# Performance work log

Measured on AMD Instinct MI355X. Metric: run time of the kernel, lower is better.

The kernel has to match this reference:

```python
import jax, jax.numpy as jnp
import numpy as np

N_TOKENS = 262144
IN_DIM = 512
NUM_EXPERTS = 64
D_E = 64
TOP_K = 2
EPS = 1e-12  # torch F.normalize eps


def _l2norm(x, axis):
    n = jnp.linalg.norm(x, axis=axis, keepdims=True)
    return x / jnp.maximum(n, EPS)


def setup_inputs() -> dict:
    key = jax.random.key(0)
    k_h, k_w, k_e, k_svd = jax.random.split(key, 4)
    h = jax.random.normal(k_h, (N_TOKENS, IN_DIM), dtype=jnp.float32)
    # xavier_uniform for W [d_e, in_dim]
    limit = float(np.sqrt(6.0 / (D_E + IN_DIM)))
    W = jax.random.uniform(k_w, (D_E, IN_DIM), minval=-limit, maxval=limit, dtype=jnp.float32)
    # orthonormal expert embeddings (SVD of random matrix), scaled by init_expert_norm=0.1
    M = jax.random.normal(k_svd, (D_E, D_E), dtype=jnp.float32)
    U, _, _ = jnp.linalg.svd(M)
    expert_embeddings = U[:NUM_EXPERTS, :] * 0.1
    tau = jnp.array(1.0, dtype=jnp.float32)
    return {"h": h, "W": W, "expert_embeddings": expert_embeddings, "tau": tau}


def reference(h, W, expert_embeddings, tau):
    # projection: [N, d_e]
    h_proj = h @ W.T
    h_norm = _l2norm(h_proj, axis=1)
    e_norm = _l2norm(expert_embeddings, axis=1)
    # cosine scores: [N, E]
    scores = h_norm @ e_norm.T
    full_gates = jax.nn.softmax(scores / tau, axis=1)
    topk_values, topk_indices = jax.lax.top_k(full_gates, TOP_K)
    normalized_topk = jax.nn.softmax(topk_values, axis=1)
    rows = jnp.arange(full_gates.shape[0])[:, None]
    sparse_gates = jnp.zeros_like(full_gates).at[rows, topk_indices].set(normalized_topk)
    return sparse_gates, topk_indices, full_gates
```

## Files before the change

kernel.cpp:

```cpp
#include <hip/hip_runtime.h>
#include <math.h>

#define NT 262144
#define KD 512
#define NE 64
#define DE 64

constexpr int BM = 128;
constexpr int NS = KD / 32;
constexpr int WS_EN = 49152;
constexpr int LD2 = 68;

using f32x4 = __attribute__((ext_vector_type(4))) float;
using s16x8 = __attribute__((ext_vector_type(8))) short;

typedef const __attribute__((address_space(1))) unsigned int* gp1_t;
typedef __attribute__((address_space(3))) unsigned int* lp3_t;

__device__ __forceinline__ void split8(float4 lo, float4 hi,
                                       s16x8& o1, s16x8& o2, s16x8& o3) {
    float x[8] = {lo.x, lo.y, lo.z, lo.w, hi.x, hi.y, hi.z, hi.w};
    union { unsigned int u[4]; s16x8 v; } r1, r2, r3;
    #pragma unroll
    for (int p = 0; p < 4; ++p) {
        float f0 = x[2 * p], f1 = x[2 * p + 1];
        unsigned int a = __float_as_uint(f0), b = __float_as_uint(f1);
        unsigned int a1 = a & 0xFFFF0000u, b1 = b & 0xFFFF0000u;
        r1.u[p] = (a1 >> 16) | b1;
        float q0 = f0 - __uint_as_float(a1);
        float q1 = f1 - __uint_as_float(b1);
        unsigned int a2 = __float_as_uint(q0) & 0xFFFF0000u;
        unsigned int b2 = __float_as_uint(q1) & 0xFFFF0000u;
        r2.u[p] = (a2 >> 16) | b2;
        float s0 = q0 - __uint_as_float(a2);
        float s1 = q1 - __uint_as_float(b2);
        r3.u[p] = (__float_as_uint(s0) >> 16) | (__float_as_uint(s1) & 0xFFFF0000u);
    }
    o1 = r1.v; o2 = r2.v; o3 = r3.v;
}

__device__ __forceinline__ s16x8 ld_frag(const unsigned int* p) {
    union { uint4 q; s16x8 v; } u;
    u.q = *(const uint4*)p;
    return u.v;
}

__global__ void prep(const float* __restrict__ W, const float* __restrict__ E,
                     unsigned int* __restrict__ ws) {
    const int tid = threadIdx.x;
    if (blockIdx.x < 16) {
        const int idx = blockIdx.x * 256 + tid;
        const int row = idx >> 6, k8 = idx & 63;
        const float* src = W + (size_t)row * KD + k8 * 8;
        float4 lo = *(const float4*)src, hi = *(const float4*)(src + 4);
        s16x8 o1, o2, o3;
        split8(lo, hi, o1, o2, o3);
        union { s16x8 v; uint4 q; } u1, u2, u3;
        u1.v = o1; u2.v = o2; u3.v = o3;
        const int ks = k8 >> 2, lk = k8 & 3, ct = row >> 4, lr = row & 15;
        const int g = ks * 4 + ct, lane = lk * 16 + lr;
        unsigned int* base = ws + (size_t)g * 768 + lane * 4;
        *(uint4*)(base)       = u1.q;
        *(uint4*)(base + 256) = u2.q;
        *(uint4*)(base + 512) = u3.q;
    } else {
        const int er = tid >> 2, part = tid & 3;
        float ss = 0.f;
        float4 ev[4];
        #pragma unroll
        for (int u = 0; u < 4; ++u) {
            ev[u] = *(const float4*)(E + er * DE + part * 16 + u * 4);
            ss = fmaf(ev[u].x, ev[u].x, ss);
            ss = fmaf(ev[u].y, ev[u].y, ss);
            ss = fmaf(ev[u].z, ev[u].z, ss);
            ss = fmaf(ev[u].w, ev[u].w, ss);
        }
        ss += __shfl_xor(ss, 1, 64);
        ss += __shfl_xor(ss, 2, 64);
        const float inv_e = 1.0f / fmaxf(sqrtf(ss), 1e-12f);
        #pragma unroll
        for (int u = 0; u < 4; ++u) {
            ev[u].x *= inv_e; ev[u].y *= inv_e; ev[u].z *= inv_e; ev[u].w *= inv_e;
        }
        #pragma unroll
        for (int half = 0; half < 2; ++half) {
            const int d0 = part * 16 + half * 8;
            s16x8 o1, o2, o3;
            split8(ev[half * 2], ev[half * 2 + 1], o1, o2, o3);
            union { s16x8 v; uint4 q; } u1, u2, u3;
            u1.v = o1; u2.v = o2; u3.v = o3;
            const int k2 = d0 >> 5, kg = (d0 >> 3) & 3;
            const int ge = k2 * 4 + (er >> 4), l = (er & 15) | (kg << 4);
            unsigned int* base = ws + WS_EN + (size_t)ge * 768 + l * 4;
            *(uint4*)(base)       = u1.q;
            *(uint4*)(base + 256) = u2.q;
            *(uint4*)(base + 512) = u3.q;
        }
    }
}

__global__ __launch_bounds__(256, 4) void moe_all(const float* __restrict__ h,
                                                  const unsigned int* __restrict__ wsW,
                                                  const float* __restrict__ tau_p,
                                                  float* __restrict__ out) {
    __shared__ float smem[10240];

    const int tid = threadIdx.x;
    const int lane = tid & 63;
    const int wv = tid >> 6;
    const int lr = lane & 15;
    const int lk = lane >> 4;
    const long tok0 = (long)blockIdx.x * BM;

    f32x4 acc[2][4];
    #pragma unroll
    for (int rt = 0; rt < 2; ++rt)
        #pragma unroll
        for (int ct = 0; ct < 4; ++ct)
            acc[rt][ct] = (f32x4){0.f, 0.f, 0.f, 0.f};

#define STAGE_A(KS)                                                            \
    {                                                                          \
        _Pragma("unroll")                                                      \
        for (int n = 0; n < 4; ++n) {                                          \
            const int flat = (wv * 4 + n) * 64 + lane;                         \
            const int t = flat >> 3, q = flat & 7;                             \
            const int qs = q ^ (t & 7);                                        \
            const float* g = h + (tok0 + t) * (long)KD + (KS) * 32 + qs * 4;   \
            float* l = smem + 6144 + wv * 1024 + n * 256;                      \
            __builtin_amdgcn_global_load_lds((gp1_t)(const void*)g,            \
                                             (lp3_t)(void*)l, 16, 0, 0);       \
        }                                                                      \
    }

#define STAGE_B(CUR, KS)                                                       \
    {                                                                          \
        _Pragma("unroll")                                                      \
        for (int i = 0; i < 3; ++i) {                                          \
            const unsigned int* g = wsW + (size_t)(KS) * 3072 + i * 1024       \
                                    + wv * 256 + lane * 4;                     \
            float* l = smem + (CUR) * 3072 + i * 1024 + wv * 256;              \
            __builtin_amdgcn_global_load_lds((gp1_t)(const void*)g,            \
                                             (lp3_t)(void*)l, 16, 0, 0);       \
        }                                                                      \
    }

    STAGE_B(0, 0);
    STAGE_A(0);

    const int sw = lr & 7;
    const int q0 = (lk * 2) ^ sw;
    const int q1 = (lk * 2 + 1) ^ sw;
    const float* abase = smem + 6144 + wv * 1024;

    for (int ks = 0; ks < NS; ++ks) {
        const int cur = ks & 1;
        asm volatile("s_waitcnt vmcnt(0)" ::: "memory");
        __builtin_amdgcn_s_barrier();
        if (ks + 1 < NS) { STAGE_B(cur ^ 1, ks + 1); }
        __builtin_amdgcn_sched_barrier(0);

        float4 xl0 = *(const float4*)(abase + lr * 32 + q0 * 4);
        float4 xh0 = *(const float4*)(abase + lr * 32 + q1 * 4);
        float4 xl1 = *(const float4*)(abase + (lr + 16) * 32 + q0 * 4);
        float4 xh1 = *(const float4*)(abase + (lr + 16) * 32 + q1 * 4);
        asm volatile("s_waitcnt lgkmcnt(0)" ::: "memory");
        if (ks + 1 < NS) { STAGE_A(ks + 1); }
        __builtin_amdgcn_sched_barrier(0);

        s16x8 a1[2], a2[2], a3[2];
        split8(xl0, xh0, a1[0], a2[0], a3[0]);
        split8(xl1, xh1, a1[1], a2[1], a3[1]);

        #pragma unroll
        for (int ct = 0; ct < 4; ++ct) {
            const unsigned int* bb =
                (const unsigned int*)(smem + cur * 3072 + ct * 768) + lane * 4;
            s16x8 b1 = ld_frag(bb);
            s16x8 b2 = ld_frag(bb + 256);
            s16x8 b3 = ld_frag(bb + 512);
            f32x4 c0 = acc[0][ct], c1 = acc[1][ct];
            c0 = __builtin_amdgcn_mfma_f32_16x16x32_bf16(a1[0], b1, c0, 0, 0, 0);
            c1 = __builtin_amdgcn_mfma_f32_16x16x32_bf16(a1[1], b1, c1, 0, 0, 0);
            c0 = __builtin_amdgcn_mfma_f32_16x16x32_bf16(a2[0], b1, c0, 0, 0, 0);
            c1 = __builtin_amdgcn_mfma_f32_16x16x32_bf16(a2[1], b1, c1, 0, 0, 0);
            c0 = __builtin_amdgcn_mfma_f32_16x16x32_bf16(a1[0], b2, c0, 0, 0, 0);
            c1 = __builtin_amdgcn_mfma_f32_16x16x32_bf16(a1[1], b2, c1, 0, 0, 0);
            c0 = __builtin_amdgcn_mfma_f32_16x16x32_bf16(a3[0], b1, c0, 0, 0, 0);
            c1 = __builtin_amdgcn_mfma_f32_16x16x32_bf16(a3[1], b1, c1, 0, 0, 0);
            c0 = __builtin_amdgcn_mfma_f32_16x16x32_bf16(a2[0], b2, c0, 0, 0, 0);
            c1 = __builtin_amdgcn_mfma_f32_16x16x32_bf16(a2[1], b2, c1, 0, 0, 0);
            c0 = __builtin_amdgcn_mfma_f32_16x16x32_bf16(a1[0], b3, c0, 0, 0, 0);
            c1 = __builtin_amdgcn_mfma_f32_16x16x32_bf16(a1[1], b3, c1, 0, 0, 0);
            acc[0][ct] = c0; acc[1][ct] = c1;
        }
    }

    float inv_n[2][4];
    #pragma unroll
    for (int rt = 0; rt < 2; ++rt) {
        #pragma unroll
        for (int r = 0; r < 4; ++r) {
            float ss = 0.f;
            #pragma unroll
            for (int ct = 0; ct < 4; ++ct)
                ss = fmaf(acc[rt][ct][r], acc[rt][ct][r], ss);
            ss += __shfl_xor(ss, 1, 64);
            ss += __shfl_xor(ss, 2, 64);
            ss += __shfl_xor(ss, 4, 64);
            ss += __shfl_xor(ss, 8, 64);
            inv_n[rt][r] = 1.0f / fmaxf(sqrtf(ss), 1e-12f);
        }
    }

    __syncthreads();

    #pragma unroll
    for (int rt = 0; rt < 2; ++rt)
        #pragma unroll
        for (int ct = 0; ct < 4; ++ct)
            #pragma unroll
            for (int r = 0; r < 4; ++r) {
                const int t = wv * 32 + rt * 16 + lk * 4 + r;
                smem[t * LD2 + ct * 16 + lr] = acc[rt][ct][r] * inv_n[rt][r];
            }

    const unsigned int* wsE = wsW + WS_EN;
    f32x4 sc[2][4];
    #pragma unroll
    for (int rt = 0; rt < 2; ++rt)
        #pragma unroll
        for (int ce = 0; ce < 4; ++ce)
            sc[rt][ce] = (f32x4){0.f, 0.f, 0.f, 0.f};

    #pragma unroll
    for (int k2 = 0; k2 < 2; ++k2) {
        s16x8 ha1[2], ha2[2], ha3[2];
        #pragma unroll
        for (int rt = 0; rt < 2; ++rt) {
            const float* ra = smem + (wv * 32 + rt * 16 + lr) * LD2 + k2 * 32 + lk * 8;
            float4 lo = *(const float4*)ra;
            float4 hi = *(const float4*)(ra + 4);
            split8(lo, hi, ha1[rt], ha2[rt], ha3[rt]);
        }
        #pragma unroll
        for (int ce = 0; ce < 4; ++ce) {
            const unsigned int* bb = wsE + (k2 * 4 + ce) * 768 + lane * 4;
            s16x8 b1 = ld_frag(bb);
            s16x8 b2 = ld_frag(bb + 256);
            s16x8 b3 = ld_frag(bb + 512);
            #pragma unroll
            for (int rt = 0; rt < 2; ++rt) {
                f32x4 c = sc[rt][ce];
                c = __builtin_amdgcn_mfma_f32_16x16x32_bf16(ha1[rt], b1, c, 0, 0, 0);
                c = __builtin_amdgcn_mfma_f32_16x16x32_bf16(ha2[rt], b1, c, 0, 0, 0);
                c = __builtin_amdgcn_mfma_f32_16x16x32_bf16(ha1[rt], b2, c, 0, 0, 0);
                c = __builtin_amdgcn_mfma_f32_16x16x32_bf16(ha3[rt], b1, c, 0, 0, 0);
                c = __builtin_amdgcn_mfma_f32_16x16x32_bf16(ha2[rt], b2, c, 0, 0, 0);
                c = __builtin_amdgcn_mfma_f32_16x16x32_bf16(ha1[rt], b3, c, 0, 0, 0);
                sc[rt][ce] = c;
            }
        }
    }

    const float inv_tau = 1.0f / tau_p[0];
    float* outS = out;
    float* outI = out + (size_t)NT * 64;
    float* outF = out + (size_t)NT * 66;

    #pragma unroll
    for (int rt = 0; rt < 2; ++rt) {
        #pragma unroll
        for (int r = 0; r < 4; ++r) {
            const long tok = tok0 + wv * 32 + rt * 16 + lk * 4 + r;
            float s[4];
            #pragma unroll
            for (int ce = 0; ce < 4; ++ce) s[ce] = sc[rt][ce][r] * inv_tau;

            float m = fmaxf(fmaxf(s[0], s[1]), fmaxf(s[2], s[3]));
            m = fmaxf(m, __shfl_xor(m, 1, 64));
            m = fmaxf(m, __shfl_xor(m, 2, 64));
            m = fmaxf(m, __shfl_xor(m, 4, 64));
            m = fmaxf(m, __shfl_xor(m, 8, 64));

            float g[4], z = 0.f;
            #pragma unroll
            for (int ce = 0; ce < 4; ++ce) { g[ce] = __expf(s[ce] - m); z += g[ce]; }
            z += __shfl_xor(z, 1, 64);
            z += __shfl_xor(z, 2, 64);
            z += __shfl_xor(z, 4, 64);
            z += __shfl_xor(z, 8, 64);
            const float invZ = 1.0f / z;

            #pragma unroll
            for (int ce = 0; ce < 4; ++ce)
                outF[tok * 64 + ce * 16 + lr] = g[ce] * invZ;

            float v1 = -3.4e38f, v2 = -3.4e38f;
            int i1 = 1 << 20, i2 = 1 << 20;
            #pragma unroll
            for (int ce = 0; ce < 4; ++ce) {
                float v = s[ce];
                int e = ce * 16 + lr;
                if (v > v1 || (v == v1 && e < i1)) { v2 = v1; i2 = i1; v1 = v; i1 = e; }
                else if (v > v2 || (v == v2 && e < i2)) { v2 = v; i2 = e; }
            }
            #pragma unroll
            for (int msk = 1; msk <= 8; msk <<= 1) {
                float o1 = __shfl_xor(v1, msk, 64); int oi1 = __shfl_xor(i1, msk, 64);
                float o2 = __shfl_xor(v2, msk, 64); int oi2 = __shfl_xor(i2, msk, 64);
                if (o1 > v1 || (o1 == v1 && oi1 < i1)) {
                    if (v1 > o2 || (v1 == o2 && i1 < oi2)) { v2 = v1; i2 = i1; }
                    else { v2 = o2; i2 = oi2; }
                    v1 = o1; i1 = oi1;
                } else {
                    if (o1 > v2 || (o1 == v2 && oi1 < i2)) { v2 = o1; i2 = oi1; }
                }
            }

            float gv1 = __expf(v1 - m) * invZ;
            float gv2 = __expf(v2 - m) * invZ;
            float qq = __expf(gv2 - gv1);
            float w1 = 1.0f / (1.0f + qq);
            float w2 = qq * w1;

            #pragma unroll
            for (int ce = 0; ce < 4; ++ce) {
                int e = ce * 16 + lr;
                outS[tok * 64 + e] = (e == i1) ? w1 : ((e == i2) ? w2 : 0.0f);
            }
            if (lr == 0) {
                *(float2*)(outI + tok * 2) = make_float2((float)i1, (float)i2);
            }
        }
    }
#undef STAGE_A
#undef STAGE_B
}

extern "C" void kernel_launch(void* const* d_in, const int* in_sizes, int n_in,
                              void* d_out, int out_size, void* d_ws, size_t ws_size,
                              hipStream_t stream) {
    const float* h   = (const float*)d_in[0];
    const float* W   = (const float*)d_in[1];
    const float* E   = (const float*)d_in[2];
    const float* tau = (const float*)d_in[3];
    float* out = (float*)d_out;
    unsigned int* ws = (unsigned int*)d_ws;

    prep<<<17, 256, 0, stream>>>(W, E, ws);
    moe_all<<<NT / BM, 256, 0, stream>>>(h, ws, tau, out);
}
```

Before: 170.2 us.

## Single-buffer W tiles and reuse LDS per wave to raise occupancy

The W-fragment stage goes from double-buffered to single-buffered, with a second barrier before each refill, and the loop is rewritten as macro phases with finer vmcnt waits. The normalized projection is staged through a small per-wave LDS region in two halves, so shared memory drops from 40 KB to 28 KB and launch bounds rise from 4 to 5 blocks per CU. It also adds s_setprio around the MFMA blocks and hoists the tau load to kernel start. The intent is better latency hiding through higher occupancy, at the cost of an extra barrier per K step and less overlap of W loads. The padded stride of 33 also makes the float4 LDS reads misaligned.

```diff
diff --git a/kernel.cpp b/kernel.cpp
--- a/kernel.cpp
+++ b/kernel.cpp
@@ -9,7 +9,7 @@
 constexpr int BM = 128;
 constexpr int NS = KD / 32;
 constexpr int WS_EN = 49152;
-constexpr int LD2 = 68;
+constexpr int LT = 33;
 
 using f32x4 = __attribute__((ext_vector_type(4))) float;
 using s16x8 = __attribute__((ext_vector_type(8))) short;
@@ -99,11 +99,11 @@
     }
 }
 
-__global__ __launch_bounds__(256, 4) void moe_all(const float* __restrict__ h,
+__global__ __launch_bounds__(256, 5) void moe_all(const float* __restrict__ h,
                                                   const unsigned int* __restrict__ wsW,
                                                   const float* __restrict__ tau_p,
                                                   float* __restrict__ out) {
-    __shared__ float smem[10240];
+    __shared__ float smem[7168];
 
     const int tid = threadIdx.x;
     const int lane = tid & 63;
@@ -111,6 +111,9 @@
     const int lr = lane & 15;
     const int lk = lane >> 4;
     const long tok0 = (long)blockIdx.x * BM;
+
+    const float inv_tau_pre = 1.0f / tau_p[0];
+    asm volatile("s_waitcnt vmcnt(0)" ::: "memory");
 
     f32x4 acc[2][4];
     #pragma unroll
@@ -127,74 +130,81 @@
             const int t = flat >> 3, q = flat & 7;                             \
             const int qs = q ^ (t & 7);                                        \
             const float* g = h + (tok0 + t) * (long)KD + (KS) * 32 + qs * 4;   \
-            float* l = smem + 6144 + wv * 1024 + n * 256;                      \
+            float* l = smem + 3072 + wv * 1024 + n * 256;                      \
             __builtin_amdgcn_global_load_lds((gp1_t)(const void*)g,            \
                                              (lp3_t)(void*)l, 16, 0, 0);       \
         }                                                                      \
     }
 
-#define STAGE_B(CUR, KS)                                                       \
+#define STAGE_B(KS)                                                            \
     {                                                                          \
         _Pragma("unroll")                                                      \
         for (int i = 0; i < 3; ++i) {                                          \
             const unsigned int* g = wsW + (size_t)(KS) * 3072 + i * 1024       \
                                     + wv * 256 + lane * 4;                     \
-            float* l = smem + (CUR) * 3072 + i * 1024 + wv * 256;              \
+            float* l = smem + i * 1024 + wv * 256;                             \
             __builtin_amdgcn_global_load_lds((gp1_t)(const void*)g,            \
                                              (lp3_t)(void*)l, 16, 0, 0);       \
         }                                                                      \
     }
 
-    STAGE_B(0, 0);
+#define PHASE(KS, LAST)                                                        \
+    {                                                                          \
+        asm volatile("s_waitcnt vmcnt(3)" ::: "memory");     \
+        float4 xl0 = *(const float4*)(abase + lr * 32 + q0 * 4);               \
+        float4 xh0 = *(const float4*)(abase + lr * 32 + q1 * 4);               \
+        float4 xl1 = *(const float4*)(abase + (lr + 16) * 32 + q0 * 4);        \
+        float4 xh1 = *(const float4*)(abase + (lr + 16) * 32 + q1 * 4);        \
+        asm volatile("s_waitcnt lgkmcnt(0)" ::: "memory");     \
+        if (!(LAST)) { STAGE_A((KS) + 1); }                                    \
+        __builtin_amdgcn_sched_barrier(0);                                     \
+        s16x8 a1[2], a2[2], a3[2];                                             \
+        split8(xl0, xh0, a1[0], a2[0], a3[0]);                                 \
+        split8(xl1, xh1, a1[1], a2[1], a3[1]);                                 \
+        if (LAST) { asm volatile("s_waitcnt vmcnt(0)" ::: "memory"); }         \
+        else      { asm volatile("s_waitcnt vmcnt(4)" ::: "memory"); }         \
+        __builtin_amdgcn_s_barrier();             \
+        __builtin_amdgcn_s_setprio(1);                                         \
+        _Pragma("unroll")                                                      \
+        for (int ct = 0; ct < 4; ++ct) {                                       \
+            const unsigned int* bb =                                           \
+                (const unsigned int*)(smem + ct * 768) + lane * 4;             \
+            s16x8 b1 = ld_frag(bb);                                            \
+            s16x8 b2 = ld_frag(bb + 256);                                      \
+            s16x8 b3 = ld_frag(bb + 512);                                      \
+            f32x4 c0 = acc[0][ct], c1 = acc[1][ct];                            \
+            c0 = __builtin_amdgcn_mfma_f32_16x16x32_bf16(a1[0], b1, c0, 0, 0, 0); \
+            c1 = __builtin_amdgcn_mfma_f32_16x16x32_bf16(a1[1], b1, c1, 0, 0, 0); \
+            c0 = __builtin_amdgcn_mfma_f32_16x16x32_bf16(a2[0], b1, c0, 0, 0, 0); \
+            c1 = __builtin_amdgcn_mfma_f32_16x16x32_bf16(a2[1], b1, c1, 0, 0, 0); \
+            c0 = __builtin_amdgcn_mfma_f32_16x16x32_bf16(a1[0], b2, c0, 0, 0, 0); \
+            c1 = __builtin_amdgcn_mfma_f32_16x16x32_bf16(a1[1], b2, c1, 0, 0, 0); \
+            c0 = __builtin_amdgcn_mfma_f32_16x16x32_bf16(a3[0], b1, c0, 0, 0, 0); \
+            c1 = __builtin_amdgcn_mfma_f32_16x16x32_bf16(a3[1], b1, c1, 0, 0, 0); \
+            c0 = __builtin_amdgcn_mfma_f32_16x16x32_bf16(a2[0], b2, c0, 0, 0, 0); \
+            c1 = __builtin_amdgcn_mfma_f32_16x16x32_bf16(a2[1], b2, c1, 0, 0, 0); \
+            c0 = __builtin_amdgcn_mfma_f32_16x16x32_bf16(a1[0], b3, c0, 0, 0, 0); \
+            c1 = __builtin_amdgcn_mfma_f32_16x16x32_bf16(a1[1], b3, c1, 0, 0, 0); \
+            acc[0][ct] = c0; acc[1][ct] = c1;                                  \
+        }                                                                      \
+        __builtin_amdgcn_s_setprio(0);                                         \
+        if (!(LAST)) {                                                         \
+            __builtin_amdgcn_s_barrier();        \
+            STAGE_B((KS) + 1);                          \
+        }                                                                      \
+    }
+
     STAGE_A(0);
+    STAGE_B(0);
+    __builtin_amdgcn_sched_barrier(0);
 
     const int sw = lr & 7;
     const int q0 = (lk * 2) ^ sw;
     const int q1 = (lk * 2 + 1) ^ sw;
-    const float* abase = smem + 6144 + wv * 1024;
-
-    for (int ks = 0; ks < NS; ++ks) {
-        const int cur = ks & 1;
-        asm volatile("s_waitcnt vmcnt(0)" ::: "memory");
-        __builtin_amdgcn_s_barrier();
-        if (ks + 1 < NS) { STAGE_B(cur ^ 1, ks + 1); }
-        __builtin_amdgcn_sched_barrier(0);
-
-        float4 xl0 = *(const float4*)(abase + lr * 32 + q0 * 4);
-        float4 xh0 = *(const float4*)(abase + lr * 32 + q1 * 4);
-        float4 xl1 = *(const float4*)(abase + (lr + 16) * 32 + q0 * 4);
-        float4 xh1 = *(const float4*)(abase + (lr + 16) * 32 + q1 * 4);
-        asm volatile("s_waitcnt lgkmcnt(0)" ::: "memory");
-        if (ks + 1 < NS) { STAGE_A(ks + 1); }
-        __builtin_amdgcn_sched_barrier(0);
-
-        s16x8 a1[2], a2[2], a3[2];
-        split8(xl0, xh0, a1[0], a2[0], a3[0]);
-        split8(xl1, xh1, a1[1], a2[1], a3[1]);
-
-        #pragma unroll
-        for (int ct = 0; ct < 4; ++ct) {
-            const unsigned int* bb =
-                (const unsigned int*)(smem + cur * 3072 + ct * 768) + lane * 4;
-            s16x8 b1 = ld_frag(bb);
-            s16x8 b2 = ld_frag(bb + 256);
-            s16x8 b3 = ld_frag(bb + 512);
-            f32x4 c0 = acc[0][ct], c1 = acc[1][ct];
-            c0 = __builtin_amdgcn_mfma_f32_16x16x32_bf16(a1[0], b1, c0, 0, 0, 0);
-            c1 = __builtin_amdgcn_mfma_f32_16x16x32_bf16(a1[1], b1, c1, 0, 0, 0);
-            c0 = __builtin_amdgcn_mfma_f32_16x16x32_bf16(a2[0], b1, c0, 0, 0, 0);
-            c1 = __builtin_amdgcn_mfma_f32_16x16x32_bf16(a2[1], b1, c1, 0, 0, 0);
-            c0 = __builtin_amdgcn_mfma_f32_16x16x32_bf16(a1[0], b2, c0, 0, 0, 0);
-            c1 = __builtin_amdgcn_mfma_f32_16x16x32_bf16(a1[1], b2, c1, 0, 0, 0);
-            c0 = __builtin_amdgcn_mfma_f32_16x16x32_bf16(a3[0], b1, c0, 0, 0, 0);
-            c1 = __builtin_amdgcn_mfma_f32_16x16x32_bf16(a3[1], b1, c1, 0, 0, 0);
-            c0 = __builtin_amdgcn_mfma_f32_16x16x32_bf16(a2[0], b2, c0, 0, 0, 0);
-            c1 = __builtin_amdgcn_mfma_f32_16x16x32_bf16(a2[1], b2, c1, 0, 0, 0);
-            c0 = __builtin_amdgcn_mfma_f32_16x16x32_bf16(a1[0], b3, c0, 0, 0, 0);
-            c1 = __builtin_amdgcn_mfma_f32_16x16x32_bf16(a1[1], b3, c1, 0, 0, 0);
-            acc[0][ct] = c0; acc[1][ct] = c1;
-        }
-    }
+    const float* abase = smem + 3072 + wv * 1024;
+
+    for (int ks = 0; ks < NS - 1; ++ks) { PHASE(ks, 0); }
+    PHASE(NS - 1, 1);
 
     float inv_n[2][4];
     #pragma unroll
@@ -215,17 +225,8 @@
 
     __syncthreads();
 
-    #pragma unroll
-    for (int rt = 0; rt < 2; ++rt)
-        #pragma unroll
-        for (int ct = 0; ct < 4; ++ct)
-            #pragma unroll
-            for (int r = 0; r < 4; ++r) {
-                const int t = wv * 32 + rt * 16 + lk * 4 + r;
-                smem[t * LD2 + ct * 16 + lr] = acc[rt][ct][r] * inv_n[rt][r];
-            }
-
     const unsigned int* wsE = wsW + WS_EN;
+    float* wreg = smem + wv * 1056;
     f32x4 sc[2][4];
     #pragma unroll
     for (int rt = 0; rt < 2; ++rt)
@@ -235,14 +236,25 @@
 
     #pragma unroll
     for (int k2 = 0; k2 < 2; ++k2) {
+        #pragma unroll
+        for (int rt = 0; rt < 2; ++rt)
+            #pragma unroll
+            for (int cl = 0; cl < 2; ++cl)
+                #pragma unroll
+                for (int r = 0; r < 4; ++r) {
+                    const int ct = k2 * 2 + cl;
+                    wreg[(rt * 16 + lk * 4 + r) * LT + cl * 16 + lr] =
+                        acc[rt][ct][r] * inv_n[rt][r];
+                }
         s16x8 ha1[2], ha2[2], ha3[2];
         #pragma unroll
         for (int rt = 0; rt < 2; ++rt) {
-            const float* ra = smem + (wv * 32 + rt * 16 + lr) * LD2 + k2 * 32 + lk * 8;
+            const float* ra = wreg + (rt * 16 + lr) * LT + lk * 8;
             float4 lo = *(const float4*)ra;
             float4 hi = *(const float4*)(ra + 4);
             split8(lo, hi, ha1[rt], ha2[rt], ha3[rt]);
         }
+        __builtin_amdgcn_s_setprio(1);
         #pragma unroll
         for (int ce = 0; ce < 4; ++ce) {
             const unsigned int* bb = wsE + (k2 * 4 + ce) * 768 + lane * 4;
@@ -261,9 +273,10 @@
                 sc[rt][ce] = c;
             }
         }
-    }
-
-    const float inv_tau = 1.0f / tau_p[0];
+        __builtin_amdgcn_s_setprio(0);
+    }
+
+    const float inv_tau = inv_tau_pre;
     float* outS = out;
     float* outI = out + (size_t)NT * 64;
     float* outF = out + (size_t)NT * 66;
@@ -336,6 +349,7 @@
     }
 #undef STAGE_A
 #undef STAGE_B
+#undef PHASE
 }
 
 extern "C" void kernel_launch(void* const* d_in, const int* in_sizes, int n_in,
```

Result: slower. 191.5 us (+12.5%).

## Replace 3-term bf16 split emulation with scaled 2-term fp16 split

Applied to the files above, without the earlier changes.

Replaces the six-MFMA bf16x3 emulation of fp32 matmul with a two-part fp16 split (hi plus residual scaled by 4096), using three fp16 MFMAs into two accumulators that are combined afterwards. This cuts MFMA count by half, shrinks the staged weight workspace and shared memory, and reduces the split-conversion ALU work. The trade-off is precision: fp16 has a narrower exponent range, so accuracy depends on input magnitudes (e.g. tiny or large values in h) staying within fp16 range.

```diff
diff --git a/kernel.cpp b/kernel.cpp
--- a/kernel.cpp
+++ b/kernel.cpp
@@ -1,4 +1,5 @@
 #include <hip/hip_runtime.h>
+#include <hip/hip_fp16.h>
 #include <math.h>
 
 #define NT 262144
@@ -8,39 +9,36 @@
 
 constexpr int BM = 128;
 constexpr int NS = KD / 32;
-constexpr int WS_EN = 49152;
+constexpr int WS_EN = 32768;
 constexpr int LD2 = 68;
+constexpr float RSC  = 4096.0f;
+constexpr float IRSC = 1.0f / 4096.0f;
 
 using f32x4 = __attribute__((ext_vector_type(4))) float;
-using s16x8 = __attribute__((ext_vector_type(8))) short;
+using f16x8 = __attribute__((ext_vector_type(8))) _Float16;
 
 typedef const __attribute__((address_space(1))) unsigned int* gp1_t;
 typedef __attribute__((address_space(3))) unsigned int* lp3_t;
 
-__device__ __forceinline__ void split8(float4 lo, float4 hi,
-                                       s16x8& o1, s16x8& o2, s16x8& o3) {
+__device__ __forceinline__ void splitf16(float4 lo, float4 hi,
+                                         f16x8& o1, f16x8& o2) {
     float x[8] = {lo.x, lo.y, lo.z, lo.w, hi.x, hi.y, hi.z, hi.w};
-    union { unsigned int u[4]; s16x8 v; } r1, r2, r3;
+    union { unsigned int u[4]; f16x8 v; } r1, r2;
     #pragma unroll
     for (int p = 0; p < 4; ++p) {
         float f0 = x[2 * p], f1 = x[2 * p + 1];
-        unsigned int a = __float_as_uint(f0), b = __float_as_uint(f1);
-        unsigned int a1 = a & 0xFFFF0000u, b1 = b & 0xFFFF0000u;
-        r1.u[p] = (a1 >> 16) | b1;
-        float q0 = f0 - __uint_as_float(a1);
-        float q1 = f1 - __uint_as_float(b1);
-        unsigned int a2 = __float_as_uint(q0) & 0xFFFF0000u;
-        unsigned int b2 = __float_as_uint(q1) & 0xFFFF0000u;
-        r2.u[p] = (a2 >> 16) | b2;
-        float s0 = q0 - __uint_as_float(a2);
-        float s1 = q1 - __uint_as_float(b2);
-        r3.u[p] = (__float_as_uint(s0) >> 16) | (__float_as_uint(s1) & 0xFFFF0000u);
-    }
-    o1 = r1.v; o2 = r2.v; o3 = r3.v;
-}
-
-__device__ __forceinline__ s16x8 ld_frag(const unsigned int* p) {
-    union { uint4 q; s16x8 v; } u;
+        __half2 h1 = __float22half2_rn(make_float2(f0, f1));
+        float2 bk = __half22float2(h1);
+        __half2 h2 = __float22half2_rn(make_float2((f0 - bk.x) * RSC,
+                                                   (f1 - bk.y) * RSC));
+        r1.u[p] = *reinterpret_cast<unsigned int*>(&h1);
+        r2.u[p] = *reinterpret_cast<unsigned int*>(&h2);
+    }
+    o1 = r1.v; o2 = r2.v;
+}
+
+__device__ __forceinline__ f16x8 ld_frag(const unsigned int* p) {
+    union { uint4 q; f16x8 v; } u;
     u.q = *(const uint4*)p;
     return u.v;
 }
@@ -53,16 +51,15 @@
         const int row = idx >> 6, k8 = idx & 63;
         const float* src = W + (size_t)row * KD + k8 * 8;
         float4 lo = *(const float4*)src, hi = *(const float4*)(src + 4);
-        s16x8 o1, o2, o3;
-        split8(lo, hi, o1, o2, o3);
-        union { s16x8 v; uint4 q; } u1, u2, u3;
-        u1.v = o1; u2.v = o2; u3.v = o3;
+        f16x8 o1, o2;
+        splitf16(lo, hi, o1, o2);
+        union { f16x8 v; uint4 q; } u1, u2;
+        u1.v = o1; u2.v = o2;
         const int ks = k8 >> 2, lk = k8 & 3, ct = row >> 4, lr = row & 15;
         const int g = ks * 4 + ct, lane = lk * 16 + lr;
-        unsigned int* base = ws + (size_t)g * 768 + lane * 4;
+        unsigned int* base = ws + (size_t)g * 512 + lane * 4;
         *(uint4*)(base)       = u1.q;
         *(uint4*)(base + 256) = u2.q;
-        *(uint4*)(base + 512) = u3.q;
     } else {
         const int er = tid >> 2, part = tid & 3;
         float ss = 0.f;
@@ -85,16 +82,15 @@
         #pragma unroll
         for (int half = 0; half < 2; ++half) {
             const int d0 = part * 16 + half * 8;
-            s16x8 o1, o2, o3;
-            split8(ev[half * 2], ev[half * 2 + 1], o1, o2, o3);
-            union { s16x8 v; uint4 q; } u1, u2, u3;
-            u1.v = o1; u2.v = o2; u3.v = o3;
+            f16x8 o1, o2;
+            splitf16(ev[half * 2], ev[half * 2 + 1], o1, o2);
+            union { f16x8 v; uint4 q; } u1, u2;
+            u1.v = o1; u2.v = o2;
             const int k2 = d0 >> 5, kg = (d0 >> 3) & 3;
             const int ge = k2 * 4 + (er >> 4), l = (er & 15) | (kg << 4);
-            unsigned int* base = ws + WS_EN + (size_t)ge * 768 + l * 4;
+            unsigned int* base = ws + WS_EN + (size_t)ge * 512 + l * 4;
             *(uint4*)(base)       = u1.q;
             *(uint4*)(base + 256) = u2.q;
-            *(uint4*)(base + 512) = u3.q;
         }
     }
 }
@@ -103,7 +99,7 @@
                                                   const unsigned int* __restrict__ wsW,
                                                   const float* __restrict__ tau_p,
                                                   float* __restrict__ out) {
-    __shared__ float smem[10240];
+    __shared__ float smem[8704];
 
     const int tid = threadIdx.x;
     const int lane = tid & 63;
@@ -112,12 +108,14 @@
     const int lk = lane >> 4;
     const long tok0 = (long)blockIdx.x * BM;
 
-    f32x4 acc[2][4];
+    f32x4 acc[2][4], ac2[2][4];
     #pragma unroll
     for (int rt = 0; rt < 2; ++rt)
         #pragma unroll
-        for (int ct = 0; ct < 4; ++ct)
+        for (int ct = 0; ct < 4; ++ct) {
             acc[rt][ct] = (f32x4){0.f, 0.f, 0.f, 0.f};
+            ac2[rt][ct] = (f32x4){0.f, 0.f, 0.f, 0.f};
+        }
 
 #define STAGE_A(KS)                                                            \
     {                                                                          \
@@ -127,7 +125,7 @@
             const int t = flat >> 3, q = flat & 7;                             \
             const int qs = q ^ (t & 7);                                        \
             const float* g = h + (tok0 + t) * (long)KD + (KS) * 32 + qs * 4;   \
-            float* l = smem + 6144 + wv * 1024 + n * 256;                      \
+            float* l = smem + 4096 + wv * 1024 + n * 256;                      \
             __builtin_amdgcn_global_load_lds((gp1_t)(const void*)g,            \
                                              (lp3_t)(void*)l, 16, 0, 0);       \
         }                                                                      \
@@ -136,10 +134,10 @@
 #define STAGE_B(CUR, KS)                                                       \
     {                                                                          \
         _Pragma("unroll")                                                      \
-        for (int i = 0; i < 3; ++i) {                                          \
-            const unsigned int* g = wsW + (size_t)(KS) * 3072 + i * 1024       \
+        for (int i = 0; i < 2; ++i) {                                          \
+            const unsigned int* g = wsW + (size_t)(KS) * 2048 + i * 1024       \
                                     + wv * 256 + lane * 4;                     \
-            float* l = smem + (CUR) * 3072 + i * 1024 + wv * 256;              \
+            float* l = smem + (CUR) * 2048 + i * 1024 + wv * 256;              \
             __builtin_amdgcn_global_load_lds((gp1_t)(const void*)g,            \
                                              (lp3_t)(void*)l, 16, 0, 0);       \
         }                                                                      \
@@ -151,7 +149,7 @@
     const int sw = lr & 7;
     const int q0 = (lk * 2) ^ sw;
     const int q1 = (lk * 2 + 1) ^ sw;
-    const float* abase = smem + 6144 + wv * 1024;
+    const float* abase = smem + 4096 + wv * 1024;
 
     for (int ks = 0; ks < NS; ++ks) {
         const int cur = ks & 1;
@@ -168,33 +166,36 @@
         if (ks + 1 < NS) { STAGE_A(ks + 1); }
         __builtin_amdgcn_sched_barrier(0);
 
-        s16x8 a1[2], a2[2], a3[2];
-        split8(xl0, xh0, a1[0], a2[0], a3[0]);
-        split8(xl1, xh1, a1[1], a2[1], a3[1]);
+        f16x8 a1[2], a2[2];
+        splitf16(xl0, xh0, a1[0], a2[0]);
+        splitf16(xl1, xh1, a1[1], a2[1]);
 
         #pragma unroll
         for (int ct = 0; ct < 4; ++ct) {
             const unsigned int* bb =
-                (const unsigned int*)(smem + cur * 3072 + ct * 768) + lane * 4;
-            s16x8 b1 = ld_frag(bb);
-            s16x8 b2 = ld_frag(bb + 256);
-            s16x8 b3 = ld_frag(bb + 512);
+                (const unsigned int*)(smem + cur * 2048) + ct * 512 + lane * 4;
+            f16x8 b1 = ld_frag(bb);
+            f16x8 b2 = ld_frag(bb + 256);
             f32x4 c0 = acc[0][ct], c1 = acc[1][ct];
-            c0 = __builtin_amdgcn_mfma_f32_16x16x32_bf16(a1[0], b1, c0, 0, 0, 0);
-            c1 = __builtin_amdgcn_mfma_f32_16x16x32_bf16(a1[1], b1, c1, 0, 0, 0);
-            c0 = __builtin_amdgcn_mfma_f32_16x16x32_bf16(a2[0], b1, c0, 0, 0, 0);
-            c1 = __builtin_amdgcn_mfma_f32_16x16x32_bf16(a2[1], b1, c1, 0, 0, 0);
-            c0 = __builtin_amdgcn_mfma_f32_16x16x32_bf16(a1[0], b2, c0, 0, 0, 0);
-            c1 = __builtin_amdgcn_mfma_f32_16x16x32_bf16(a1[1], b2, c1, 0, 0, 0);
-            c0 = __builtin_amdgcn_mfma_f32_16x16x32_bf16(a3[0], b1, c0, 0, 0, 0);
-            c1 = __builtin_amdgcn_mfma_f32_16x16x32_bf16(a3[1], b1, c1, 0, 0, 0);
-            c0 = __builtin_amdgcn_mfma_f32_16x16x32_bf16(a2[0], b2, c0, 0, 0, 0);
-            c1 = __builtin_amdgcn_mfma_f32_16x16x32_bf16(a2[1], b2, c1, 0, 0, 0);
-            c0 = __builtin_amdgcn_mfma_f32_16x16x32_bf16(a1[0], b3, c0, 0, 0, 0);
-            c1 = __builtin_amdgcn_mfma_f32_16x16x32_bf16(a1[1], b3, c1, 0, 0, 0);
+            f32x4 d0 = ac2[0][ct], d1 = ac2[1][ct];
+            c0 = __builtin_amdgcn_mfma_f32_16x16x32_f16(a1[0], b1, c0, 0, 0, 0);
+            c1 = __builtin_amdgcn_mfma_f32_16x16x32_f16(a1[1], b1, c1, 0, 0, 0);
+            d0 = __builtin_amdgcn_mfma_f32_16x16x32_f16(a1[0], b2, d0, 0, 0, 0);
+            d1 = __builtin_amdgcn_mfma_f32_16x16x32_f16(a1[1], b2, d1, 0, 0, 0);
+            d0 = __builtin_amdgcn_mfma_f32_16x16x32_f16(a2[0], b1, d0, 0, 0, 0);
+            d1 = __builtin_amdgcn_mfma_f32_16x16x32_f16(a2[1], b1, d1, 0, 0, 0);
             acc[0][ct] = c0; acc[1][ct] = c1;
-        }
-    }
+            ac2[0][ct] = d0; ac2[1][ct] = d1;
+        }
+    }
+
+    #pragma unroll
+    for (int rt = 0; rt < 2; ++rt)
+        #pragma unroll
+        for (int ct = 0; ct < 4; ++ct)
+            #pragma unroll
+            for (int r = 0; r < 4; ++r)
+                acc[rt][ct][r] = fmaf(ac2[rt][ct][r], IRSC, acc[rt][ct][r]);
 
     float inv_n[2][4];
     #pragma unroll
@@ -226,39 +227,37 @@
             }
 
     const unsigned int* wsE = wsW + WS_EN;
-    f32x4 sc[2][4];
+    f32x4 sc[2][4], sc2[2][4];
     #pragma unroll
     for (int rt = 0; rt < 2; ++rt)
         #pragma unroll
-        for (int ce = 0; ce < 4; ++ce)
-            sc[rt][ce] = (f32x4){0.f, 0.f, 0.f, 0.f};
+        for (int ce = 0; ce < 4; ++ce) {
+            sc[rt][ce]  = (f32x4){0.f, 0.f, 0.f, 0.f};
+            sc2[rt][ce] = (f32x4){0.f, 0.f, 0.f, 0.f};
+        }
 
     #pragma unroll
     for (int k2 = 0; k2 < 2; ++k2) {
-        s16x8 ha1[2], ha2[2], ha3[2];
+        f16x8 ha1[2], ha2[2];
         #pragma unroll
         for (int rt = 0; rt < 2; ++rt) {
             const float* ra = smem + (wv * 32 + rt * 16 + lr) * LD2 + k2 * 32 + lk * 8;
             float4 lo = *(const float4*)ra;
             float4 hi = *(const float4*)(ra + 4);
-            split8(lo, hi, ha1[rt], ha2[rt], ha3[rt]);
+            splitf16(lo, hi, ha1[rt], ha2[rt]);
         }
         #pragma unroll
         for (int ce = 0; ce < 4; ++ce) {
-            const unsigned int* bb = wsE + (k2 * 4 + ce) * 768 + lane * 4;
-            s16x8 b1 = ld_frag(bb);
-            s16x8 b2 = ld_frag(bb + 256);
-            s16x8 b3 = ld_frag(bb + 512);
+            const unsigned int* bb = wsE + (k2 * 4 + ce) * 512 + lane * 4;
+            f16x8 b1 = ld_frag(bb);
+            f16x8 b2 = ld_frag(bb + 256);
             #pragma unroll
             for (int rt = 0; rt < 2; ++rt) {
-                f32x4 c = sc[rt][ce];
-                c = __builtin_amdgcn_mfma_f32_16x16x32_bf16(ha1[rt], b1, c, 0, 0, 0);
-                c = __builtin_amdgcn_mfma_f32_16x16x32_bf16(ha2[rt], b1, c, 0, 0, 0);
-                c = __builtin_amdgcn_mfma_f32_16x16x32_bf16(ha1[rt], b2, c, 0, 0, 0);
-                c = __builtin_amdgcn_mfma_f32_16x16x32_bf16(ha3[rt], b1, c, 0, 0, 0);
-                c = __builtin_amdgcn_mfma_f32_16x16x32_bf16(ha2[rt], b2, c, 0, 0, 0);
-                c = __builtin_amdgcn_mfma_f32_16x16x32_bf16(ha1[rt], b3, c, 0, 0, 0);
-                sc[rt][ce] = c;
+                f32x4 c = sc[rt][ce], d = sc2[rt][ce];
+                c = __builtin_amdgcn_mfma_f32_16x16x32_f16(ha1[rt], b1, c, 0, 0, 0);
+                d = __builtin_amdgcn_mfma_f32_16x16x32_f16(ha1[rt], b2, d, 0, 0, 0);
+                d = __builtin_amdgcn_mfma_f32_16x16x32_f16(ha2[rt], b1, d, 0, 0, 0);
+                sc[rt][ce] = c; sc2[rt][ce] = d;
             }
         }
     }
@@ -275,7 +274,8 @@
             const long tok = tok0 + wv * 32 + rt * 16 + lk * 4 + r;
             float s[4];
             #pragma unroll
-            for (int ce = 0; ce < 4; ++ce) s[ce] = sc[rt][ce][r] * inv_tau;
+            for (int ce = 0; ce < 4; ++ce)
+                s[ce] = fmaf(sc2[rt][ce][r], IRSC, sc[rt][ce][r]) * inv_tau;
 
             float m = fmaxf(fmaxf(s[0], s[1]), fmaxf(s[2], s[3]));
             m = fmaxf(m, __shfl_xor(m, 1, 64));
```

After: 160.2 us. 1.06x faster.
